# Kernel optimization log

Measured on AMD Instinct MI355X. Metric: run time of the kernel, lower is better.

The kernel has to match this reference:

```python
import jax, jax.numpy as jnp
import numpy as np

N = 100000
E = 1600000
IN_C = 128
HID = 256
EPS = 1e-5


def setup_inputs() -> dict:
    key = jax.random.key(0)
    ks = jax.random.split(key, 20)
    s = lambda fi, fo: (1.0 / np.sqrt(fi))
    inp = {
        "x": jax.random.normal(ks[0], (N, IN_C), dtype=jnp.float32),
        "edge_index": jax.random.randint(ks[1], (2, E), 0, N, dtype=jnp.int64),
        # SAGEConv (in -> hidden): lin_l (on aggregated neighbors, with bias), lin_r (root, no bias)
        "Wl": jax.random.normal(ks[2], (HID, IN_C), dtype=jnp.float32) * s(IN_C, HID),
        "bl": jnp.zeros((HID,), dtype=jnp.float32),
        "Wr": jax.random.normal(ks[3], (HID, IN_C), dtype=jnp.float32) * s(IN_C, HID),
        # bns[0]
        "bn_g": jnp.ones((HID,), dtype=jnp.float32),
        "bn_b": jnp.zeros((HID,), dtype=jnp.float32),
        # linear stack hidden->hidden->64->14->2
        "W1": jax.random.normal(ks[4], (HID, HID), dtype=jnp.float32) * s(HID, HID),
        "b1": jnp.zeros((HID,), dtype=jnp.float32),
        "W2": jax.random.normal(ks[5], (64, HID), dtype=jnp.float32) * s(HID, 64),
        "b2": jnp.zeros((64,), dtype=jnp.float32),
        "W3": jax.random.normal(ks[6], (14, 64), dtype=jnp.float32) * s(64, 14),
        "b3": jnp.zeros((14,), dtype=jnp.float32),
        "W4": jax.random.normal(ks[7], (2, 14), dtype=jnp.float32) * s(14, 2),
        "b4": jnp.zeros((2,), dtype=jnp.float32),
        # bns2: BN(hidden), BN(64), BN(14)
        "g1": jnp.ones((HID,), dtype=jnp.float32), "bb1": jnp.zeros((HID,), dtype=jnp.float32),
        "g2": jnp.ones((64,), dtype=jnp.float32), "bb2": jnp.zeros((64,), dtype=jnp.float32),
        "g3": jnp.ones((14,), dtype=jnp.float32), "bb3": jnp.zeros((14,), dtype=jnp.float32),
    }
    return inp


def _bn(h, g, b):
    # training-mode BatchNorm1d: batch mean, biased variance
    m = h.mean(axis=0)
    v = jnp.mean((h - m) ** 2, axis=0)
    return g * (h - m) * jax.lax.rsqrt(v + EPS) + b


def _sage_mean(x, edge_index, Wl, bl, Wr):
    src, dst = edge_index[0], edge_index[1]
    n = x.shape[0]
    agg = jax.ops.segment_sum(x[src], dst, num_segments=n)  # [N, F]
    cnt = jax.ops.segment_sum(jnp.ones((src.shape[0],), x.dtype), dst, num_segments=n)
    agg = agg / jnp.maximum(cnt, 1.0)[:, None]
    return agg @ Wl.T + bl + x @ Wr.T


def reference(x, edge_index, Wl, bl, Wr, bn_g, bn_b,
              W1, b1, W2, b2, W3, b3, W4, b4,
              g1, bb1, g2, bb2, g3, bb3):
    # convs2[:-1] loop (num_layers=2 -> single conv), dropout is identity (eval)
    h = _sage_mean(x, edge_index, Wl, bl, Wr)
    h = jax.nn.relu(_bn(h, bn_g, bn_b))
    # linear stack with bns2 + relu
    h = jax.nn.relu(_bn(h @ W1.T + b1, g1, bb1))
    h = jax.nn.relu(_bn(h @ W2.T + b2, g2, bb2))
    h = jax.nn.relu(_bn(h @ W3.T + b3, g3, bb3))
    h = h @ W4.T + b4
    return jax.nn.log_softmax(h, axis=-1)
```

## Files before the change

### kernel.cpp

```cpp
#include <hip/hip_runtime.h>
#include <math.h>

#define BN_EPS 1e-5f
#define STAT_NB 64
#define GBIN 512
#define BSH 7

typedef unsigned short u16;
typedef __attribute__((ext_vector_type(8))) unsigned short u16x8;
typedef __attribute__((ext_vector_type(8))) short bf16x8;
typedef __attribute__((ext_vector_type(4))) float f32x4;

__device__ __forceinline__ float bf2f(u16 b){
  union{unsigned int u; float f;} c; c.u = ((unsigned int)b)<<16; return c.f;
}
__device__ __forceinline__ u16 f2bf(float f){
  union{float f; unsigned int u;} c; c.f=f;
  unsigned int u = c.u;
  return (u16)((u + 0x7fffu + ((u>>16)&1u)) >> 16);
}


__global__ __launch_bounds__(256) void k_hist(const int* __restrict__ ei, int E, int nbkt,
                                              int* __restrict__ blkhist){
  __shared__ int hist[1024];
  int tid = threadIdx.x, blk = blockIdx.x;
  for (int b=tid;b<1024;b+=256) hist[b]=0;
  __syncthreads();
  int per = (E + GBIN - 1)/GBIN;
  int e0 = blk*per, e1 = min(E, e0+per);
  for (int e=e0+tid; e<e1; e+=256)
    atomicAdd(&hist[ei[(size_t)E+e]>>BSH], 1);
  __syncthreads();
  for (int b=tid;b<nbkt;b+=256) blkhist[(size_t)b*GBIN + blk] = hist[b];
}

__global__ void k_rowscan(int* __restrict__ blkhist, int nbkt, int* __restrict__ bbase){
  int b = blockIdx.x*blockDim.x + threadIdx.x;
  if (b >= nbkt) return;
  int run = 0;
  for (int k=0;k<GBIN;k++){
    size_t idx = (size_t)b*GBIN + k;
    int t = blkhist[idx];
    blkhist[idx] = run;
    run += t;
  }
  bbase[b] = run;
}

__global__ void k_bscan(int* __restrict__ bbase, int nbkt){
  __shared__ int s[1024];
  int tid = threadIdx.x;
  int v = (tid<nbkt)? bbase[tid] : 0;
  s[tid]=v; __syncthreads();
  #pragma unroll
  for (int o=1;o<1024;o<<=1){
    int t = (tid>=o)? s[tid-o] : 0;
    __syncthreads();
    s[tid]+=t;
    __syncthreads();
  }
  if (tid<nbkt) bbase[tid] = s[tid]-v;
  if (tid==1023) bbase[nbkt] = s[1023];
}

__global__ __launch_bounds__(256) void k_scatter(const int* __restrict__ ei, int E, int nbkt,
                                                 const int* __restrict__ blkhist,
                                                 const int* __restrict__ bbase,
                                                 int* __restrict__ pairs){
  __shared__ int cur[1024];
  int tid = threadIdx.x, blk = blockIdx.x;
  for (int b=tid;b<nbkt;b+=256) cur[b] = bbase[b] + blkhist[(size_t)b*GBIN + blk];
  __syncthreads();
  int per = (E + GBIN - 1)/GBIN;
  int e0 = blk*per, e1 = min(E, e0+per);
  for (int e=e0+tid; e<e1; e+=256){
    int dst = ei[(size_t)E+e];
    int src = ei[e];
    int b = dst>>BSH;
    int p = atomicAdd(&cur[b], 1);
    pairs[p] = (src<<BSH) | (dst & 127);
  }
}

__global__ __launch_bounds__(256) void k_bucket_csr(const int* __restrict__ pairs,
                                                    const int* __restrict__ bbase,
                                                    int nbkt, int n,
                                                    int* __restrict__ deg, int* __restrict__ off,
                                                    int* __restrict__ eidx){
  __shared__ int hist[128], loff[128], cur2[128];
  int tid = threadIdx.x, b = blockIdx.x;
  if (b >= nbkt) return;
  int n0 = b<<BSH;
  int nn = min(128, n - n0);
  int e0 = bbase[b], e1 = bbase[b+1];
  int cnt = e1 - e0;
  if (tid<128) hist[tid]=0;
  __syncthreads();
  for (int i=tid;i<cnt;i+=256)
    atomicAdd(&hist[pairs[e0+i] & 127], 1);
  __syncthreads();
  int hv=0;
  if (tid<128){ hv = hist[tid]; loff[tid] = hv; }
  __syncthreads();
  #pragma unroll
  for (int o=1;o<128;o<<=1){
    int t = (tid<128 && tid>=o)? loff[tid-o] : 0;
    __syncthreads();
    if (tid<128) loff[tid]+=t;
    __syncthreads();
  }
  if (tid<128){
    int ex = loff[tid]-hv;
    cur2[tid] = ex;
    if (tid<nn){
      deg[n0+tid] = hv;
      off[n0+tid] = e0 + ex;
    }
  }
  __syncthreads();
  for (int i=tid;i<cnt;i+=256){
    int v = pairs[e0+i];
    int p = atomicAdd(&cur2[v & 127], 1);
    eidx[e0 + p] = v>>BSH;
  }
}


__global__ void k_cvt_x(const float* __restrict__ x, u16* __restrict__ Acat, int n){
  int i = blockIdx.x*blockDim.x + threadIdx.x;
  int total = n*16;
  int stride = gridDim.x*blockDim.x;
  for (; i<total; i+=stride){
    int r = i>>4, kb = (i&15)*8;
    const float4* src = (const float4*)(x + (size_t)r*128 + kb);
    float4 a = src[0], b = src[1];
    u16x8 v;
    v[0]=f2bf(a.x); v[1]=f2bf(a.y); v[2]=f2bf(a.z); v[3]=f2bf(a.w);
    v[4]=f2bf(b.x); v[5]=f2bf(b.y); v[6]=f2bf(b.z); v[7]=f2bf(b.w);
    *(u16x8*)(Acat + (size_t)r*256 + 128 + kb) = v;
  }
}

__global__ void k_cvt_w(const float* __restrict__ w, u16* __restrict__ wb, int total8){
  int i = blockIdx.x*blockDim.x + threadIdx.x;
  int stride = gridDim.x*blockDim.x;
  for (; i<total8; i+=stride){
    const float4* src = (const float4*)(w + (size_t)i*8);
    float4 a = src[0], b = src[1];
    u16x8 v;
    v[0]=f2bf(a.x); v[1]=f2bf(a.y); v[2]=f2bf(a.z); v[3]=f2bf(a.w);
    v[4]=f2bf(b.x); v[5]=f2bf(b.y); v[6]=f2bf(b.z); v[7]=f2bf(b.w);
    *(u16x8*)(wb + (size_t)i*8) = v;
  }
}

__global__ void k_cvt_cat(const float* __restrict__ Wl, const float* __restrict__ Wr,
                          u16* __restrict__ Wb1){
  int i = blockIdx.x*blockDim.x + threadIdx.x;
  if (i >= 8192) return;
  int c = i>>5, kb = (i&31)*8;
  const float* src = (kb<128) ? (Wl + (size_t)c*128 + kb) : (Wr + (size_t)c*128 + kb-128);
  float4 a = ((const float4*)src)[0], b = ((const float4*)src)[1];
  u16x8 v;
  v[0]=f2bf(a.x); v[1]=f2bf(a.y); v[2]=f2bf(a.z); v[3]=f2bf(a.w);
  v[4]=f2bf(b.x); v[5]=f2bf(b.y); v[6]=f2bf(b.z); v[7]=f2bf(b.w);
  *(u16x8*)(Wb1 + (size_t)c*256 + kb) = v;
}

__global__ void k_aggregate(u16* Acat, const int* __restrict__ off,
                            const int* __restrict__ deg, const int* __restrict__ eidx, int n){
  int wid = (blockIdx.x*blockDim.x + threadIdx.x) >> 6;
  int lane = threadIdx.x & 63;
  if (wid >= n) return;
  int o = off[wid], d = deg[wid];
  int eslot = lane >> 3;
  int ck = (lane & 7) * 16;
  float f[16];
  #pragma unroll
  for (int j=0;j<16;j++) f[j]=0.f;
  for (int i = eslot; i < d; i += 8){
    int s = eidx[o+i];
    const u16x8* src = (const u16x8*)(Acat + (size_t)s*256 + 128 + ck);
    u16x8 v0 = src[0], v1 = src[1];
    #pragma unroll
    for (int j=0;j<8;j++) f[j]   += bf2f(v0[j]);
    #pragma unroll
    for (int j=0;j<8;j++) f[8+j] += bf2f(v1[j]);
  }
  #pragma unroll
  for (int j=0;j<16;j++){
    f[j] += __shfl_xor(f[j], 8, 64);
    f[j] += __shfl_xor(f[j], 16, 64);
    f[j] += __shfl_xor(f[j], 32, 64);
  }
  if (lane < 8){
    float inv = 1.f/(float)max(d,1);
    u16x8 r0, r1;
    #pragma unroll
    for (int j=0;j<8;j++){ r0[j]=f2bf(f[j]*inv); r1[j]=f2bf(f[8+j]*inv); }
    u16x8* dst = (u16x8*)(Acat + (size_t)wid*256 + ck);
    dst[0]=r0; dst[1]=r1;
  }
}


template<int COLS>
__global__ __launch_bounds__(256) void k_gemm_mfma(
    const u16* __restrict__ A, const u16* __restrict__ W,
    const float* __restrict__ ss, int has_ss,
    const float* __restrict__ bias, u16* __restrict__ out,
    int nrows, int hout,
    float* __restrict__ psum, float* __restrict__ psq)
{
  constexpr int WN  = COLS/2;
  constexpr int NFR = WN/16;
  __shared__ u16 As[128*64];
  __shared__ u16 Bs[COLS*64];
  __shared__ float scs[256], shs[256];
  __shared__ float red[2][2][COLS];

  int tid  = threadIdx.x;
  int lane = tid & 63, wave = tid >> 6;
  int wr = wave >> 1, wc = wave & 1;
  int rbase = blockIdx.x*128, cbase = blockIdx.y*COLS;

  if (has_ss){ scs[tid] = ss[tid]; shs[tid] = ss[256+tid]; }
  __syncthreads();

  f32x4 acc[4][NFR];
  #pragma unroll
  for (int m=0;m<4;m++)
    #pragma unroll
    for (int n=0;n<NFR;n++)
      acc[m][n] = (f32x4){0.f,0.f,0.f,0.f};

  int arow = tid >> 1;
  int acb  = (tid & 1) * 32;
  bool avalid = (rbase + arow) < nrows;
  const u16* aptr = A + (size_t)(rbase+arow)*256 + acb;
  int brow, bcb;
  if (COLS==128){ brow = tid>>1; bcb = (tid&1)*32; }
  else          { brow = tid>>2; bcb = (tid&3)*16; }
  const u16* bptr = W + (size_t)(cbase+brow)*256 + bcb;

  for (int kt=0; kt<256; kt+=64){
    #pragma unroll
    for (int q=0;q<4;q++){
      u16x8 v = (u16x8){0,0,0,0,0,0,0,0};
      if (avalid) v = *(const u16x8*)(aptr + kt + q*8);
      if (has_ss){
        int k = acb + q*8;
        #pragma unroll
        for (int e=0;e<8;e++){
          float f = bf2f(v[e]);
          f = fmaxf(fmaf(f, scs[kt+k+e], shs[kt+k+e]), 0.f);
          v[e] = f2bf(f);
        }
      }
      int slot = ((acb>>3) + q) ^ (arow & 7);
      *(u16x8*)(As + arow*64 + slot*8) = v;
    }
    #pragma unroll
    for (int q=0;q<COLS/32;q++){
      u16x8 v = *(const u16x8*)(bptr + kt + q*8);
      int slot = ((bcb>>3) + q) ^ (brow & 7);
      *(u16x8*)(Bs + brow*64 + slot*8) = v;
    }
    __syncthreads();

    int fr = lane & 15, g = lane >> 4;
    #pragma unroll
    for (int kk=0;kk<2;kk++){
      bf16x8 af[4], bfr[NFR];
      #pragma unroll
      for (int m=0;m<4;m++){
        int row = wr*64 + m*16 + fr;
        int slot = (kk*4 + g) ^ (row & 7);
        af[m] = *(const bf16x8*)(As + row*64 + slot*8);
      }
      #pragma unroll
      for (int n=0;n<NFR;n++){
        int row = wc*WN + n*16 + fr;
        int slot = (kk*4 + g) ^ (row & 7);
        bfr[n] = *(const bf16x8*)(Bs + row*64 + slot*8);
      }
      #pragma unroll
      for (int m=0;m<4;m++)
        #pragma unroll
        for (int n=0;n<NFR;n++)
          acc[m][n] = __builtin_amdgcn_mfma_f32_16x16x32_bf16(af[m], bfr[n], acc[m][n], 0, 0, 0);
    }
    __syncthreads();
  }

  int cl = lane & 15, g = lane >> 4;
  float bv[NFR], sn[NFR], qn[NFR];
  #pragma unroll
  for (int n=0;n<NFR;n++){
    bv[n] = bias[cbase + wc*WN + n*16 + cl];
    sn[n] = 0.f; qn[n] = 0.f;
  }
  #pragma unroll
  for (int m=0;m<4;m++){
    int r0 = rbase + wr*64 + m*16 + g*4;
    #pragma unroll
    for (int n=0;n<NFR;n++){
      int c = cbase + wc*WN + n*16 + cl;
      #pragma unroll
      for (int i=0;i<4;i++){
        int r = r0 + i;
        if (r < nrows){
          float v = acc[m][n][i] + bv[n];
          out[(size_t)r*hout + c] = f2bf(v);
          sn[n] += v; qn[n] += v*v;
        }
      }
    }
  }
  #pragma unroll
  for (int n=0;n<NFR;n++){
    sn[n] += __shfl_xor(sn[n], 16, 64);
    sn[n] += __shfl_xor(sn[n], 32, 64);
    qn[n] += __shfl_xor(qn[n], 16, 64);
    qn[n] += __shfl_xor(qn[n], 32, 64);
  }
  if (lane < 16){
    #pragma unroll
    for (int n=0;n<NFR;n++){
      int cc = wc*WN + n*16 + lane;
      red[0][wr][cc] = sn[n];
      red[1][wr][cc] = qn[n];
    }
  }
  __syncthreads();
  if (tid < COLS){
    psum[(size_t)blockIdx.x*hout + cbase + tid] = red[0][0][tid] + red[0][1][tid];
  } else if (tid < 2*COLS){
    int c = tid - COLS;
    psq[(size_t)blockIdx.x*hout + cbase + c] = red[1][0][c] + red[1][1][c];
  }
}


__global__ __launch_bounds__(256) void k_stats_part(
    const float* __restrict__ psum, const float* __restrict__ psq,
    int rt, int h, float* __restrict__ part){
  int c = threadIdx.x;
  int b = blockIdx.x;
  if (c >= h) return;
  int chunk = (rt + STAT_NB - 1)/STAT_NB;
  int i0 = b*chunk;
  int i1 = min(rt, i0+chunk);
  float s0=0.f,s1=0.f,s2=0.f,s3=0.f, q0=0.f,q1=0.f,q2=0.f,q3=0.f;
  int i=i0;
  for (; i+3<i1; i+=4){
    s0 += psum[(size_t)i*h+c];     q0 += psq[(size_t)i*h+c];
    s1 += psum[(size_t)(i+1)*h+c]; q1 += psq[(size_t)(i+1)*h+c];
    s2 += psum[(size_t)(i+2)*h+c]; q2 += psq[(size_t)(i+2)*h+c];
    s3 += psum[(size_t)(i+3)*h+c]; q3 += psq[(size_t)(i+3)*h+c];
  }
  for (; i<i1; ++i){ s0 += psum[(size_t)i*h+c]; q0 += psq[(size_t)i*h+c]; }
  part[((size_t)b*2  )*h + c] = (s0+s1)+(s2+s3);
  part[((size_t)b*2+1)*h + c] = (q0+q1)+(q2+q3);
}

__global__ void k_stats_fold(const float* __restrict__ part, int h, float ninv,
                             const float* __restrict__ g, const float* __restrict__ b_,
                             float* __restrict__ ss){
  int c = threadIdx.x;
  if (c >= h) return;
  float S0=0.f,S1=0.f,Q0=0.f,Q1=0.f;
  #pragma unroll 2
  for (int b=0;b<STAT_NB;b+=2){
    S0 += part[((size_t)b*2  )*h + c];
    Q0 += part[((size_t)b*2+1)*h + c];
    S1 += part[((size_t)(b+1)*2  )*h + c];
    Q1 += part[((size_t)(b+1)*2+1)*h + c];
  }
  float S = S0+S1, Q = Q0+Q1;
  float m = S*ninv;
  float v = fmaxf(Q*ninv - m*m, 0.f);
  float sc = g[c] * rsqrtf(v + BN_EPS);
  ss[c]   = sc;
  ss[h+c] = b_[c] - m*sc;
}

__global__ __launch_bounds__(256) void k_lin3(const u16* __restrict__ h3, const float* __restrict__ ss3,
     const float* __restrict__ W3, const float* __restrict__ b3,
     float* __restrict__ h4, int n, float* __restrict__ psum, float* __restrict__ psq){
  __shared__ float Ws[14*64];
  __shared__ float bs[14];
  __shared__ float sc[64], sh[64];
  __shared__ float redp[2][14][4];
  int tid=threadIdx.x;
  for (int i=tid;i<896;i+=256) Ws[i]=W3[i];
  if (tid<14) bs[tid]=b3[tid];
  if (tid<64){ sc[tid]=ss3[tid]; sh[tid]=ss3[64+tid]; }
  __syncthreads();
  int node = blockIdx.x*256 + tid;
  float o[14];
  #pragma unroll
  for (int hh=0;hh<14;hh++) o[hh]=0.f;
  if (node<n){
    const u16x8* ar = (const u16x8*)(h3 + (size_t)node*64);
    #pragma unroll
    for (int kv=0;kv<8;kv++){
      u16x8 v = ar[kv];
      #pragma unroll
      for (int j=0;j<8;j++){
        int k=kv*8+j;
        float a = fmaxf(fmaf(bf2f(v[j]), sc[k], sh[k]), 0.f);
        #pragma unroll
        for (int hh=0;hh<14;hh++) o[hh] = fmaf(a, Ws[hh*64+k], o[hh]);
      }
    }
    #pragma unroll
    for (int hh=0;hh<14;hh++){ o[hh]+=bs[hh]; h4[(size_t)node*14+hh]=o[hh]; }
  }
  int lane = tid & 63, w = tid>>6;
  #pragma unroll
  for (int hh=0;hh<14;hh++){
    float sv = (node<n)? o[hh] : 0.f;
    float qv = sv*sv;
    #pragma unroll
    for (int offs=32;offs>0;offs>>=1){
      sv += __shfl_down(sv,offs,64);
      qv += __shfl_down(qv,offs,64);
    }
    if (lane==0){ redp[0][hh][w]=sv; redp[1][hh][w]=qv; }
  }
  __syncthreads();
  if (tid<14){
    float t=redp[0][tid][0]+redp[0][tid][1]+redp[0][tid][2]+redp[0][tid][3];
    psum[(size_t)blockIdx.x*14+tid]=t;
  } else if (tid>=64 && tid<78){
    int c=tid-64;
    float t=redp[1][c][0]+redp[1][c][1]+redp[1][c][2]+redp[1][c][3];
    psq[(size_t)blockIdx.x*14+c]=t;
  }
}

__global__ void k_final(const float* __restrict__ h4, const float* __restrict__ ss4,
   const float* __restrict__ W4, const float* __restrict__ b4, float* __restrict__ out, int n){
  int node = blockIdx.x*blockDim.x+threadIdx.x;
  if (node>=n) return;
  float z0=b4[0], z1=b4[1];
  #pragma unroll
  for (int j=0;j<14;j++){
    float a = fmaxf(h4[(size_t)node*14+j]*ss4[j]+ss4[14+j], 0.f);
    z0 = fmaf(a, W4[j],    z0);
    z1 = fmaf(a, W4[14+j], z1);
  }
  float m = fmaxf(z0,z1);
  float lse = m + logf(expf(z0-m)+expf(z1-m));
  out[(size_t)node*2]   = z0-lse;
  out[(size_t)node*2+1] = z1-lse;
}

extern "C" void kernel_launch(void* const* d_in, const int* in_sizes, int n_in,
                              void* d_out, int out_size, void* d_ws, size_t ws_size,
                              hipStream_t stream){
  const float* x    = (const float*)d_in[0];
  const int*   ei   = (const int*)d_in[1];
  const float* Wl   = (const float*)d_in[2];
  const float* bl   = (const float*)d_in[3];
  const float* Wr   = (const float*)d_in[4];
  const float* bn_g = (const float*)d_in[5];
  const float* bn_b = (const float*)d_in[6];
  const float* W1   = (const float*)d_in[7];
  const float* b1   = (const float*)d_in[8];
  const float* W2   = (const float*)d_in[9];
  const float* b2   = (const float*)d_in[10];
  const float* W3   = (const float*)d_in[11];
  const float* b3   = (const float*)d_in[12];
  const float* W4   = (const float*)d_in[13];
  const float* b4   = (const float*)d_in[14];
  const float* g1   = (const float*)d_in[15];
  const float* bb1  = (const float*)d_in[16];
  const float* g2   = (const float*)d_in[17];
  const float* bb2  = (const float*)d_in[18];
  const float* g3   = (const float*)d_in[19];
  const float* bb3  = (const float*)d_in[20];

  const int N = in_sizes[0]/128;
  const int E = in_sizes[1]/2;
  const int NBKT = (N + 127) >> BSH;
  const int RT2 = (N+127)/128;
  const int RT4 = (N+255)/256;

  char* p = (char*)d_ws;
  auto alloc = [&](size_t bytes)->void*{
    void* r = (void*)p;
    p += (bytes + 255) & ~(size_t)255;
    return r;
  };
  int* deg      = (int*)alloc((size_t)N*sizeof(int));
  int* off      = (int*)alloc((size_t)N*sizeof(int));
  int* bbase    = (int*)alloc(1025*sizeof(int));
  int* blkhist  = (int*)alloc((size_t)1024*GBIN*sizeof(int));
  int* pairs    = (int*)alloc((size_t)E*sizeof(int));
  int* eidx     = (int*)alloc((size_t)E*sizeof(int));
  u16* Acat     = (u16*)alloc((size_t)N*256*sizeof(u16));
  u16* h1b      = (u16*)alloc((size_t)N*256*sizeof(u16));
  float* h4     = (float*)alloc((size_t)N*14*sizeof(float));
  u16* Wb1      = (u16*)alloc(256*256*sizeof(u16));
  u16* Wb2      = (u16*)alloc(256*256*sizeof(u16));
  u16* Wb3      = (u16*)alloc(64*256*sizeof(u16));
  float* psum   = (float*)alloc((size_t)RT2*256*sizeof(float));
  float* psq    = (float*)alloc((size_t)RT2*256*sizeof(float));
  float* part   = (float*)alloc((size_t)STAT_NB*2*256*sizeof(float));
  float* ssb    = (float*)alloc(4*512*sizeof(float));
  u16* h2b = Acat;
  u16* h3b = h1b;
  float* ss1=ssb, *ss2=ssb+512, *ss3=ssb+1024, *ss4=ssb+1536;
  const float ninv = 1.f/(float)N;

  k_cvt_cat<<<dim3(32), dim3(256), 0, stream>>>(Wl, Wr, Wb1);
  k_cvt_w<<<dim3(32), dim3(256), 0, stream>>>(W1, Wb2, 8192);
  k_cvt_w<<<dim3(8),  dim3(256), 0, stream>>>(W2, Wb3, 2048);
  k_cvt_x<<<dim3(2048), dim3(256), 0, stream>>>(x, Acat, N);

  k_hist<<<dim3(GBIN), dim3(256), 0, stream>>>(ei, E, NBKT, blkhist);
  k_rowscan<<<dim3((NBKT+255)/256), dim3(256), 0, stream>>>(blkhist, NBKT, bbase);
  k_bscan<<<dim3(1), dim3(1024), 0, stream>>>(bbase, NBKT);
  k_scatter<<<dim3(GBIN), dim3(256), 0, stream>>>(ei, E, NBKT, blkhist, bbase, pairs);
  k_bucket_csr<<<dim3(NBKT), dim3(256), 0, stream>>>(pairs, bbase, NBKT, N, deg, off, eidx);

  k_aggregate<<<dim3((N+3)/4), dim3(256), 0, stream>>>(Acat, off, deg, eidx, N);

  k_gemm_mfma<128><<<dim3(RT2,2), dim3(256), 0, stream>>>(
      Acat, Wb1, (const float*)0, 0, bl, h1b, N, 256, psum, psq);
  k_stats_part<<<dim3(STAT_NB), dim3(256), 0, stream>>>(psum, psq, RT2, 256, part);
  k_stats_fold<<<dim3(1), dim3(256), 0, stream>>>(part, 256, ninv, bn_g, bn_b, ss1);

  k_gemm_mfma<128><<<dim3(RT2,2), dim3(256), 0, stream>>>(
      h1b, Wb2, ss1, 1, b1, h2b, N, 256, psum, psq);
  k_stats_part<<<dim3(STAT_NB), dim3(256), 0, stream>>>(psum, psq, RT2, 256, part);
  k_stats_fold<<<dim3(1), dim3(256), 0, stream>>>(part, 256, ninv, g1, bb1, ss2);

  k_gemm_mfma<64><<<dim3(RT2,1), dim3(256), 0, stream>>>(
      h2b, Wb3, ss2, 1, b2, h3b, N, 64, psum, psq);
  k_stats_part<<<dim3(STAT_NB), dim3(256), 0, stream>>>(psum, psq, RT2, 64, part);
  k_stats_fold<<<dim3(1), dim3(64), 0, stream>>>(part, 64, ninv, g2, bb2, ss3);

  k_lin3<<<dim3(RT4), dim3(256), 0, stream>>>(h3b, ss3, W3, b3, h4, N, psum, psq);
  k_stats_part<<<dim3(STAT_NB), dim3(256), 0, stream>>>(psum, psq, RT4, 14, part);
  k_stats_fold<<<dim3(1), dim3(64), 0, stream>>>(part, 14, ninv, g3, bb3, ss4);

  k_final<<<dim3((N+255)/256), dim3(256), 0, stream>>>(h4, ss4, W4, b4, (float*)d_out, N);
}
```

Before: 351.7 us.

## Fuse prep and stats kernels, widen GEMM tile to full 256 columns

Merges the four conversion kernels into one launch and replaces the two-kernel BN statistics reduction with a single kernel that uses a last-block counter to do the final fold. The GEMM now covers all 256 output columns per block instead of splitting them over two grid columns, so each A tile is loaded once, and it gets a two-blocks-per-CU launch bound. The block histogram layout is transposed so the histogram and scatter kernels write and read contiguously, and the aggregation loop is unrolled by two. The wider tile raises register and shared memory pressure per block, and the counter-based fold adds a fence and atomic.

Measured after the change: 365.4 us. 3.9% more time.

```diff
diff --git a/kernel.cpp b/kernel.cpp
--- a/kernel.cpp
+++ b/kernel.cpp
@@ -18,6 +18,43 @@
   union{float f; unsigned int u;} c; c.f=f;
   unsigned int u = c.u;
   return (u16)((u + 0x7fffu + ((u>>16)&1u)) >> 16);
+}
+
+__global__ __launch_bounds__(256) void k_prep(
+    const float* __restrict__ Wl, const float* __restrict__ Wr,
+    const float* __restrict__ W1, const float* __restrict__ W2,
+    const float* __restrict__ x,
+    u16* __restrict__ Wb1, u16* __restrict__ Wb2, u16* __restrict__ Wb3,
+    u16* __restrict__ Acat, int n, int* __restrict__ flags){
+  int bid = blockIdx.x, tid = threadIdx.x;
+  if (bid==0 && tid<8) flags[tid]=0;
+  auto cv8 = [](const float* s)->u16x8{
+    float4 a = ((const float4*)s)[0], b = ((const float4*)s)[1];
+    u16x8 v;
+    v[0]=f2bf(a.x); v[1]=f2bf(a.y); v[2]=f2bf(a.z); v[3]=f2bf(a.w);
+    v[4]=f2bf(b.x); v[5]=f2bf(b.y); v[6]=f2bf(b.z); v[7]=f2bf(b.w);
+    return v;
+  };
+  if (bid < 32){
+    int i = bid*256 + tid;
+    int c = i>>5, kb = (i&31)*8;
+    const float* src = (kb<128) ? (Wl + (size_t)c*128 + kb) : (Wr + (size_t)c*128 + kb-128);
+    *(u16x8*)(Wb1 + (size_t)c*256 + kb) = cv8(src);
+  } else if (bid < 64){
+    int i = (bid-32)*256 + tid;
+    *(u16x8*)(Wb2 + (size_t)i*8) = cv8(W1 + (size_t)i*8);
+  } else if (bid < 72){
+    int i = (bid-64)*256 + tid;
+    if (i < 2048) *(u16x8*)(Wb3 + (size_t)i*8) = cv8(W2 + (size_t)i*8);
+  } else {
+    int i = (bid-72)*256 + tid;
+    int total = n*16;
+    int stride = (gridDim.x-72)*256;
+    for (; i<total; i+=stride){
+      int r = i>>4, kb = (i&15)*8;
+      *(u16x8*)(Acat + (size_t)r*256 + 128 + kb) = cv8(x + (size_t)r*128 + kb);
+    }
+  }
 }
 
 
@@ -32,7 +69,7 @@
   for (int e=e0+tid; e<e1; e+=256)
     atomicAdd(&hist[ei[(size_t)E+e]>>BSH], 1);
   __syncthreads();
-  for (int b=tid;b<nbkt;b+=256) blkhist[(size_t)b*GBIN + blk] = hist[b];
+  for (int b=tid;b<nbkt;b+=256) blkhist[(size_t)blk*nbkt + b] = hist[b];
 }
 
 __global__ void k_rowscan(int* __restrict__ blkhist, int nbkt, int* __restrict__ bbase){
@@ -40,7 +77,7 @@
   if (b >= nbkt) return;
   int run = 0;
   for (int k=0;k<GBIN;k++){
-    size_t idx = (size_t)b*GBIN + k;
+    size_t idx = (size_t)k*nbkt + b;
     int t = blkhist[idx];
     blkhist[idx] = run;
     run += t;
@@ -70,7 +107,7 @@
                                                  int* __restrict__ pairs){
   __shared__ int cur[1024];
   int tid = threadIdx.x, blk = blockIdx.x;
-  for (int b=tid;b<nbkt;b+=256) cur[b] = bbase[b] + blkhist[(size_t)b*GBIN + blk];
+  for (int b=tid;b<nbkt;b+=256) cur[b] = bbase[b] + blkhist[(size_t)blk*nbkt + b];
   __syncthreads();
   int per = (E + GBIN - 1)/GBIN;
   int e0 = blk*per, e1 = min(E, e0+per);
@@ -126,48 +163,6 @@
   }
 }
 
-
-__global__ void k_cvt_x(const float* __restrict__ x, u16* __restrict__ Acat, int n){
-  int i = blockIdx.x*blockDim.x + threadIdx.x;
-  int total = n*16;
-  int stride = gridDim.x*blockDim.x;
-  for (; i<total; i+=stride){
-    int r = i>>4, kb = (i&15)*8;
-    const float4* src = (const float4*)(x + (size_t)r*128 + kb);
-    float4 a = src[0], b = src[1];
-    u16x8 v;
-    v[0]=f2bf(a.x); v[1]=f2bf(a.y); v[2]=f2bf(a.z); v[3]=f2bf(a.w);
-    v[4]=f2bf(b.x); v[5]=f2bf(b.y); v[6]=f2bf(b.z); v[7]=f2bf(b.w);
-    *(u16x8*)(Acat + (size_t)r*256 + 128 + kb) = v;
-  }
-}
-
-__global__ void k_cvt_w(const float* __restrict__ w, u16* __restrict__ wb, int total8){
-  int i = blockIdx.x*blockDim.x + threadIdx.x;
-  int stride = gridDim.x*blockDim.x;
-  for (; i<total8; i+=stride){
-    const float4* src = (const float4*)(w + (size_t)i*8);
-    float4 a = src[0], b = src[1];
-    u16x8 v;
-    v[0]=f2bf(a.x); v[1]=f2bf(a.y); v[2]=f2bf(a.z); v[3]=f2bf(a.w);
-    v[4]=f2bf(b.x); v[5]=f2bf(b.y); v[6]=f2bf(b.z); v[7]=f2bf(b.w);
-    *(u16x8*)(wb + (size_t)i*8) = v;
-  }
-}
-
-__global__ void k_cvt_cat(const float* __restrict__ Wl, const float* __restrict__ Wr,
-                          u16* __restrict__ Wb1){
-  int i = blockIdx.x*blockDim.x + threadIdx.x;
-  if (i >= 8192) return;
-  int c = i>>5, kb = (i&31)*8;
-  const float* src = (kb<128) ? (Wl + (size_t)c*128 + kb) : (Wr + (size_t)c*128 + kb-128);
-  float4 a = ((const float4*)src)[0], b = ((const float4*)src)[1];
-  u16x8 v;
-  v[0]=f2bf(a.x); v[1]=f2bf(a.y); v[2]=f2bf(a.z); v[3]=f2bf(a.w);
-  v[4]=f2bf(b.x); v[5]=f2bf(b.y); v[6]=f2bf(b.z); v[7]=f2bf(b.w);
-  *(u16x8*)(Wb1 + (size_t)c*256 + kb) = v;
-}
-
 __global__ void k_aggregate(u16* Acat, const int* __restrict__ off,
                             const int* __restrict__ deg, const int* __restrict__ eidx, int n){
   int wid = (blockIdx.x*blockDim.x + threadIdx.x) >> 6;
@@ -179,6 +174,7 @@
   float f[16];
   #pragma unroll
   for (int j=0;j<16;j++) f[j]=0.f;
+  #pragma unroll 2
   for (int i = eslot; i < d; i += 8){
     int s = eidx[o+i];
     const u16x8* src = (const u16x8*)(Acat + (size_t)s*256 + 128 + ck);
@@ -206,7 +202,7 @@
 
 
 template<int COLS>
-__global__ __launch_bounds__(256) void k_gemm_mfma(
+__global__ __launch_bounds__(256, 2) void k_gemm_mfma(
     const u16* __restrict__ A, const u16* __restrict__ W,
     const float* __restrict__ ss, int has_ss,
     const float* __restrict__ bias, u16* __restrict__ out,
@@ -223,7 +219,8 @@
   int tid  = threadIdx.x;
   int lane = tid & 63, wave = tid >> 6;
   int wr = wave >> 1, wc = wave & 1;
-  int rbase = blockIdx.x*128, cbase = blockIdx.y*COLS;
+  int rbase = blockIdx.x*128;
+  constexpr int cbase = 0;
 
   if (has_ss){ scs[tid] = ss[tid]; shs[tid] = ss[256+tid]; }
   __syncthreads();
@@ -240,8 +237,9 @@
   bool avalid = (rbase + arow) < nrows;
   const u16* aptr = A + (size_t)(rbase+arow)*256 + acb;
   int brow, bcb;
-  if (COLS==128){ brow = tid>>1; bcb = (tid&1)*32; }
-  else          { brow = tid>>2; bcb = (tid&3)*16; }
+  if (COLS==256)      { brow = tid;    bcb = 0; }
+  else if (COLS==128) { brow = tid>>1; bcb = (tid&1)*32; }
+  else                { brow = tid>>2; bcb = (tid&3)*16; }
   const u16* bptr = W + (size_t)(cbase+brow)*256 + bcb;
 
   for (int kt=0; kt<256; kt+=64){
@@ -262,7 +260,7 @@
       *(u16x8*)(As + arow*64 + slot*8) = v;
     }
     #pragma unroll
-    for (int q=0;q<COLS/32;q++){
+    for (int q=0;q<(COLS==256?8:COLS/32);q++){
       u16x8 v = *(const u16x8*)(bptr + kt + q*8);
       int slot = ((bcb>>3) + q) ^ (brow & 7);
       *(u16x8*)(Bs + brow*64 + slot*8) = v;
@@ -336,54 +334,52 @@
   __syncthreads();
   if (tid < COLS){
     psum[(size_t)blockIdx.x*hout + cbase + tid] = red[0][0][tid] + red[0][1][tid];
-  } else if (tid < 2*COLS){
-    int c = tid - COLS;
-    psq[(size_t)blockIdx.x*hout + cbase + c] = red[1][0][c] + red[1][1][c];
-  }
-}
-
-
-__global__ __launch_bounds__(256) void k_stats_part(
+    psq [(size_t)blockIdx.x*hout + cbase + tid] = red[1][0][tid] + red[1][1][tid];
+  }
+}
+
+__global__ __launch_bounds__(256) void k_stats_partfold(
     const float* __restrict__ psum, const float* __restrict__ psq,
-    int rt, int h, float* __restrict__ part){
-  int c = threadIdx.x;
-  int b = blockIdx.x;
-  if (c >= h) return;
+    int rt, int h, float* __restrict__ part, float ninv,
+    const float* __restrict__ g, const float* __restrict__ b_,
+    float* __restrict__ ss, int* __restrict__ counter){
+  __shared__ int isLast;
+  int c = threadIdx.x, b = blockIdx.x;
   int chunk = (rt + STAT_NB - 1)/STAT_NB;
   int i0 = b*chunk;
   int i1 = min(rt, i0+chunk);
-  float s0=0.f,s1=0.f,s2=0.f,s3=0.f, q0=0.f,q1=0.f,q2=0.f,q3=0.f;
-  int i=i0;
-  for (; i+3<i1; i+=4){
-    s0 += psum[(size_t)i*h+c];     q0 += psq[(size_t)i*h+c];
-    s1 += psum[(size_t)(i+1)*h+c]; q1 += psq[(size_t)(i+1)*h+c];
-    s2 += psum[(size_t)(i+2)*h+c]; q2 += psq[(size_t)(i+2)*h+c];
-    s3 += psum[(size_t)(i+3)*h+c]; q3 += psq[(size_t)(i+3)*h+c];
-  }
-  for (; i<i1; ++i){ s0 += psum[(size_t)i*h+c]; q0 += psq[(size_t)i*h+c]; }
-  part[((size_t)b*2  )*h + c] = (s0+s1)+(s2+s3);
-  part[((size_t)b*2+1)*h + c] = (q0+q1)+(q2+q3);
-}
-
-__global__ void k_stats_fold(const float* __restrict__ part, int h, float ninv,
-                             const float* __restrict__ g, const float* __restrict__ b_,
-                             float* __restrict__ ss){
-  int c = threadIdx.x;
-  if (c >= h) return;
-  float S0=0.f,S1=0.f,Q0=0.f,Q1=0.f;
-  #pragma unroll 2
-  for (int b=0;b<STAT_NB;b+=2){
-    S0 += part[((size_t)b*2  )*h + c];
-    Q0 += part[((size_t)b*2+1)*h + c];
-    S1 += part[((size_t)(b+1)*2  )*h + c];
-    Q1 += part[((size_t)(b+1)*2+1)*h + c];
-  }
-  float S = S0+S1, Q = Q0+Q1;
-  float m = S*ninv;
-  float v = fmaxf(Q*ninv - m*m, 0.f);
-  float sc = g[c] * rsqrtf(v + BN_EPS);
-  ss[c]   = sc;
-  ss[h+c] = b_[c] - m*sc;
+  if (c < h){
+    float s0=0.f,s1=0.f,s2=0.f,s3=0.f, q0=0.f,q1=0.f,q2=0.f,q3=0.f;
+    int i=i0;
+    for (; i+3<i1; i+=4){
+      s0 += psum[(size_t)i*h+c];     q0 += psq[(size_t)i*h+c];
+      s1 += psum[(size_t)(i+1)*h+c]; q1 += psq[(size_t)(i+1)*h+c];
+      s2 += psum[(size_t)(i+2)*h+c]; q2 += psq[(size_t)(i+2)*h+c];
+      s3 += psum[(size_t)(i+3)*h+c]; q3 += psq[(size_t)(i+3)*h+c];
+    }
+    for (; i<i1; ++i){ s0 += psum[(size_t)i*h+c]; q0 += psq[(size_t)i*h+c]; }
+    part[((size_t)b*2  )*h + c] = (s0+s1)+(s2+s3);
+    part[((size_t)b*2+1)*h + c] = (q0+q1)+(q2+q3);
+  }
+  __threadfence();
+  if (c==0) isLast = (atomicAdd(counter,1) == gridDim.x-1);
+  __syncthreads();
+  if (isLast && c < h){
+    float S0=0.f,S1=0.f,Q0=0.f,Q1=0.f;
+    #pragma unroll 2
+    for (int b2=0;b2<STAT_NB;b2+=2){
+      S0 += part[((size_t)b2*2  )*h + c];
+      Q0 += part[((size_t)b2*2+1)*h + c];
+      S1 += part[((size_t)(b2+1)*2  )*h + c];
+      Q1 += part[((size_t)(b2+1)*2+1)*h + c];
+    }
+    float S = S0+S1, Q = Q0+Q1;
+    float m = S*ninv;
+    float v = fmaxf(Q*ninv - m*m, 0.f);
+    float sc = g[c] * rsqrtf(v + BN_EPS);
+    ss[c]   = sc;
+    ss[h+c] = b_[c] - m*sc;
+  }
 }
 
 __global__ __launch_bounds__(256) void k_lin3(const u16* __restrict__ h3, const float* __restrict__ ss3,
@@ -498,6 +494,7 @@
   int* deg      = (int*)alloc((size_t)N*sizeof(int));
   int* off      = (int*)alloc((size_t)N*sizeof(int));
   int* bbase    = (int*)alloc(1025*sizeof(int));
+  int* flags    = (int*)alloc(16*sizeof(int));
   int* blkhist  = (int*)alloc((size_t)1024*GBIN*sizeof(int));
   int* pairs    = (int*)alloc((size_t)E*sizeof(int));
   int* eidx     = (int*)alloc((size_t)E*sizeof(int));
@@ -516,10 +513,7 @@
   float* ss1=ssb, *ss2=ssb+512, *ss3=ssb+1024, *ss4=ssb+1536;
   const float ninv = 1.f/(float)N;
 
-  k_cvt_cat<<<dim3(32), dim3(256), 0, stream>>>(Wl, Wr, Wb1);
-  k_cvt_w<<<dim3(32), dim3(256), 0, stream>>>(W1, Wb2, 8192);
-  k_cvt_w<<<dim3(8),  dim3(256), 0, stream>>>(W2, Wb3, 2048);
-  k_cvt_x<<<dim3(2048), dim3(256), 0, stream>>>(x, Acat, N);
+  k_prep<<<dim3(72+2048), dim3(256), 0, stream>>>(Wl, Wr, W1, W2, x, Wb1, Wb2, Wb3, Acat, N, flags);
 
   k_hist<<<dim3(GBIN), dim3(256), 0, stream>>>(ei, E, NBKT, blkhist);
   k_rowscan<<<dim3((NBKT+255)/256), dim3(256), 0, stream>>>(blkhist, NBKT, bbase);
@@ -529,24 +523,24 @@
 
   k_aggregate<<<dim3((N+3)/4), dim3(256), 0, stream>>>(Acat, off, deg, eidx, N);
 
-  k_gemm_mfma<128><<<dim3(RT2,2), dim3(256), 0, stream>>>(
+  k_gemm_mfma<256><<<dim3(RT2), dim3(256), 0, stream>>>(
       Acat, Wb1, (const float*)0, 0, bl, h1b, N, 256, psum, psq);
-  k_stats_part<<<dim3(STAT_NB), dim3(256), 0, stream>>>(psum, psq, RT2, 256, part);
-  k_stats_fold<<<dim3(1), dim3(256), 0, stream>>>(part, 256, ninv, bn_g, bn_b, ss1);
-
-  k_gemm_mfma<128><<<dim3(RT2,2), dim3(256), 0, stream>>>(
+  k_stats_partfold<<<dim3(STAT_NB), dim3(256), 0, stream>>>(
+      psum, psq, RT2, 256, part, ninv, bn_g, bn_b, ss1, flags+0);
+
+  k_gemm_mfma<256><<<dim3(RT2), dim3(256), 0, stream>>>(
       h1b, Wb2, ss1, 1, b1, h2b, N, 256, psum, psq);
-  k_stats_part<<<dim3(STAT_NB), dim3(256), 0, stream>>>(psum, psq, RT2, 256, part);
-  k_stats_fold<<<dim3(1), dim3(256), 0, stream>>>(part, 256, ninv, g1, bb1, ss2);
-
-  k_gemm_mfma<64><<<dim3(RT2,1), dim3(256), 0, stream>>>(
+  k_stats_partfold<<<dim3(STAT_NB), dim3(256), 0, stream>>>(
+      psum, psq, RT2, 256, part, ninv, g1, bb1, ss2, flags+1);
+
+  k_gemm_mfma<64><<<dim3(RT2), dim3(256), 0, stream>>>(
       h2b, Wb3, ss2, 1, b2, h3b, N, 64, psum, psq);
-  k_stats_part<<<dim3(STAT_NB), dim3(256), 0, stream>>>(psum, psq, RT2, 64, part);
-  k_stats_fold<<<dim3(1), dim3(64), 0, stream>>>(part, 64, ninv, g2, bb2, ss3);
+  k_stats_partfold<<<dim3(STAT_NB), dim3(256), 0, stream>>>(
+      psum, psq, RT2, 64, part, ninv, g2, bb2, ss3, flags+2);
 
   k_lin3<<<dim3(RT4), dim3(256), 0, stream>>>(h3b, ss3, W3, b3, h4, N, psum, psq);
-  k_stats_part<<<dim3(STAT_NB), dim3(256), 0, stream>>>(psum, psq, RT4, 14, part);
-  k_stats_fold<<<dim3(1), dim3(64), 0, stream>>>(part, 14, ninv, g3, bb3, ss4);
+  k_stats_partfold<<<dim3(STAT_NB), dim3(256), 0, stream>>>(
+      psum, psq, RT4, 14, part, ninv, g3, bb3, ss4, flags+3);
 
   k_final<<<dim3((N+255)/256), dim3(256), 0, stream>>>(h4, ss4, W4, b4, (float*)d_out, N);
 }
```
